# Kernel tuning notes

Measured on AMD Instinct MI355X. Metric: run time of the kernel, lower is better.

Reference implementation:

```python
import jax, jax.numpy as jnp
import numpy as np

N0, N1, N2 = 100000, 300000, 200000
C = 64
SLOPE = 0.2

NNZ_A0, NNZ_A1, NNZ_C2, NNZ_B1, NNZ_B2 = 600000, 1200000, 600000, 600000, 600000


def _seg_softmax(logits, seg, n):
    # softmax over nonzero entries of each row (segment = row index)
    m = jax.ops.segment_max(logits, seg, num_segments=n)
    e = jnp.exp(logits - m[seg])
    s = jax.ops.segment_sum(e, seg, num_segments=n)
    return e / s[seg]


def _hbs(x, rows, cols, W, a, n):
    # Higher-order attention block, same rank (m_hop=1, A values = 1)
    m = x @ W                                   # [n, out]
    out = W.shape[1]
    logits = jax.nn.leaky_relu((m @ a[:out])[rows] + (m @ a[out:])[cols], SLOPE)
    att = _seg_softmax(logits, rows, n)         # row-wise softmax on sparsity pattern
    return jax.ops.segment_sum(att[:, None] * m[cols], rows, num_segments=n)


def _hbns(xs, xt, t_rows, s_cols, Ws, Wt, a, n_s, n_t):
    # Higher-order attention block between ranks; neighborhood is [n_t, n_s]
    sm = xs @ Ws                                # [n_s, t_out]
    tm = xt @ Wt                                # [n_t, s_out]
    t_out, s_out = Ws.shape[1], Wt.shape[1]
    # e: source -> target attention logits (row = target); cat([sm_j, tm_i]) @ a
    e = jax.nn.leaky_relu((sm @ a[:t_out])[s_cols] + (tm @ a[t_out:])[t_rows], SLOPE)
    # f: target -> source attention logits (row = source); cat([tm_i, sm_j]) @ a
    f = jax.nn.leaky_relu((tm @ a[:s_out])[t_rows] + (sm @ a[s_out:])[s_cols], SLOPE)
    att_st = _seg_softmax(e, t_rows, n_t)
    att_ts = _seg_softmax(f, s_cols, n_s)
    msg_t = jax.ops.segment_sum(att_st[:, None] * sm[s_cols], t_rows, num_segments=n_t)
    msg_s = jax.ops.segment_sum(att_ts[:, None] * tm[t_rows], s_cols, num_segments=n_s)
    return msg_s, msg_t


def setup_inputs() -> dict:
    key = jax.random.key(0)
    ks = iter(jax.random.split(key, 64))
    sc = 1.0 / np.sqrt(C)
    d = {
        "x_0": jax.random.normal(next(ks), (N0, C), jnp.float32),
        "x_1": jax.random.normal(next(ks), (N1, C), jnp.float32),
        "x_2": jax.random.normal(next(ks), (N2, C), jnp.float32),
        "adj0_rows": jax.random.randint(next(ks), (NNZ_A0,), 0, N0, jnp.int32),
        "adj0_cols": jax.random.randint(next(ks), (NNZ_A0,), 0, N0, jnp.int32),
        "adj1_rows": jax.random.randint(next(ks), (NNZ_A1,), 0, N1, jnp.int32),
        "adj1_cols": jax.random.randint(next(ks), (NNZ_A1,), 0, N1, jnp.int32),
        "coadj2_rows": jax.random.randint(next(ks), (NNZ_C2,), 0, N2, jnp.int32),
        "coadj2_cols": jax.random.randint(next(ks), (NNZ_C2,), 0, N2, jnp.int32),
        "inc1_rows": jax.random.randint(next(ks), (NNZ_B1,), 0, N0, jnp.int32),
        "inc1_cols": jax.random.randint(next(ks), (NNZ_B1,), 0, N1, jnp.int32),
        "inc2_rows": jax.random.randint(next(ks), (NNZ_B2,), 0, N1, jnp.int32),
        "inc2_cols": jax.random.randint(next(ks), (NNZ_B2,), 0, N2, jnp.int32),
    }
    for nm in ["W_hbs0_l1", "W_hbs0_l2", "W_hbs1_l2", "W_hbs2_l2",
               "Ws01_l1", "Wt01_l1", "Ws12_l1", "Wt12_l1",
               "Ws01_l2", "Wt01_l2", "Ws12_l2", "Wt12_l2"]:
        d[nm] = jax.random.normal(next(ks), (C, C), jnp.float32) * sc
    for nm in ["a_hbs0_l1", "a_hbs0_l2", "a_hbs1_l2", "a_hbs2_l2",
               "a01_l1", "a12_l1", "a01_l2", "a12_l2"]:
        d[nm] = jax.random.normal(next(ks), (2 * C,), jnp.float32) * sc
    return d


def reference(x_0, x_1, x_2,
              adj0_rows, adj0_cols, adj1_rows, adj1_cols,
              coadj2_rows, coadj2_cols, inc1_rows, inc1_cols,
              inc2_rows, inc2_cols,
              W_hbs0_l1, a_hbs0_l1, W_hbs0_l2, a_hbs0_l2,
              W_hbs1_l2, a_hbs1_l2, W_hbs2_l2, a_hbs2_l2,
              Ws01_l1, Wt01_l1, a01_l1, Ws12_l1, Wt12_l1, a12_l1,
              Ws01_l2, Wt01_l2, a01_l2, Ws12_l2, Wt12_l2, a12_l2):
    # ---- level 1 ----
    x_0_to_0 = _hbs(x_0, adj0_rows, adj0_cols, W_hbs0_l1, a_hbs0_l1, N0)
    x_0_to_1, x_1_to_0 = _hbns(x_1, x_0, inc1_rows, inc1_cols,
                               Ws01_l1, Wt01_l1, a01_l1, N1, N0)
    x_1_to_2, x_2_to_1 = _hbns(x_2, x_1, inc2_rows, inc2_cols,
                               Ws12_l1, Wt12_l1, a12_l1, N2, N1)
    x_0_l1 = x_0_to_0 + x_1_to_0
    x_1_l1 = x_0_to_1 + x_2_to_1
    x_2_l1 = x_1_to_2
    # ---- level 2 ----
    x_0_to_0 = _hbs(x_0_l1, adj0_rows, adj0_cols, W_hbs0_l2, a_hbs0_l2, N0)
    x_1_to_1 = _hbs(x_1_l1, adj1_rows, adj1_cols, W_hbs1_l2, a_hbs1_l2, N1)
    x_2_to_2 = _hbs(x_2_l1, coadj2_rows, coadj2_cols, W_hbs2_l2, a_hbs2_l2, N2)
    x_0_to_1, _ = _hbns(x_1_l1, x_0_l1, inc1_rows, inc1_cols,
                        Ws01_l2, Wt01_l2, a01_l2, N1, N0)
    x_1_to_2, _ = _hbns(x_2_l1, x_1_l1, inc2_rows, inc2_cols,
                        Ws12_l2, Wt12_l2, a12_l2, N2, N1)
    x_0_out = x_0_to_0
    x_1_out = x_0_to_1 + x_1_to_1
    x_2_out = x_1_to_2 + x_2_to_2
    return x_0_out, x_1_out, x_2_out
```

## Files before the change

### kernel.cpp

```cpp
#include <hip/hip_runtime.h>

#define CN0 100000
#define CN1 300000
#define CN2 200000
#define EA0 600000
#define EA1 1200000
#define EC2 600000
#define EB1 600000
#define EB2 600000
#define TOTSEG (2*CN0 + 3*CN1 + 2*CN2)
#define TOTE   (EA0 + EA1 + EC2 + 2*EB1 + 2*EB2)

typedef __attribute__((ext_vector_type(8))) short short8;
typedef __attribute__((ext_vector_type(4))) float f32x4;
typedef __attribute__((ext_vector_type(4))) unsigned short u16x4;

__device__ __forceinline__ float lrelu(float v) { return v >= 0.f ? v : 0.2f * v; }
__device__ __forceinline__ unsigned short btop(float x) {
    return (unsigned short)(__float_as_uint(x) >> 16);
}
__device__ __forceinline__ unsigned short f2bf(float x) {
    unsigned u = __float_as_uint(x);
    return (unsigned short)((u + 0x7FFFu + ((u >> 16) & 1u)) >> 16);
}
__device__ __forceinline__ float bf2f(unsigned short b) {
    return __uint_as_float((unsigned)b << 16);
}

struct Pats {
    const int* seg[7];
    const int* vidx[7];
    int E[7];
    int base[7];
    int ebase[7];
};


__global__ void k_histrank(Pats P, int* __restrict__ rp1, int* __restrict__ rank) {
    int p = blockIdx.y;
    int e = blockIdx.x * blockDim.x + threadIdx.x;
    if (e >= P.E[p]) return;
    int gs = P.base[p] + P.seg[p][e];
    rank[P.ebase[p] + e] = atomicAdd(&rp1[gs], 1);
}

__global__ void k_blkscan(int* __restrict__ d, int n, int* __restrict__ bsum) {
    __shared__ int sh[256];
    int i = blockIdx.x * 256 + threadIdx.x;
    sh[threadIdx.x] = (i < n) ? d[i] : 0;
    __syncthreads();
    for (int off = 1; off < 256; off <<= 1) {
        int t = (threadIdx.x >= (unsigned)off) ? sh[threadIdx.x - off] : 0;
        __syncthreads();
        sh[threadIdx.x] += t;
        __syncthreads();
    }
    if (i < n) d[i] = sh[threadIdx.x];
    if (threadIdx.x == 255) bsum[blockIdx.x] = sh[255];
}

__global__ void k_scanb(int* __restrict__ bsum, int nb) {
    __shared__ int sh[256];
    __shared__ int carry;
    if (threadIdx.x == 0) carry = 0;
    __syncthreads();
    for (int base = 0; base < nb; base += 256) {
        int i = base + threadIdx.x;
        sh[threadIdx.x] = (i < nb) ? bsum[i] : 0;
        __syncthreads();
        for (int off = 1; off < 256; off <<= 1) {
            int t = (threadIdx.x >= (unsigned)off) ? sh[threadIdx.x - off] : 0;
            __syncthreads();
            sh[threadIdx.x] += t;
            __syncthreads();
        }
        if (i < nb) bsum[i] = sh[threadIdx.x] + carry;
        __syncthreads();
        if (threadIdx.x == 0) carry += sh[255];
        __syncthreads();
    }
}

__global__ void k_addoff(int* __restrict__ d, const int* __restrict__ bsum, int n) {
    int i = blockIdx.x * 256 + threadIdx.x;
    if (i < n && blockIdx.x > 0) d[i] += bsum[blockIdx.x - 1];
}

__global__ void k_place(Pats P, const int* __restrict__ rp, const int* __restrict__ rank,
                        int* __restrict__ vP) {
    int p = blockIdx.y;
    int e = blockIdx.x * blockDim.x + threadIdx.x;
    if (e >= P.E[p]) return;
    int gs = P.base[p] + P.seg[p][e];
    int pos = rp[gs] + rank[P.ebase[p] + e];
    vP[pos] = P.vidx[p][e];
}

__global__ void mm64_mfma(const float* __restrict__ X, const float* __restrict__ W,
                          const float* __restrict__ a, unsigned short* __restrict__ Yb,
                          float* __restrict__ p, float* __restrict__ q, int nchunk) {
    int lane = threadIdx.x & 63;
    int l15 = lane & 15, lq = lane >> 4;
    int wid = blockIdx.x * (blockDim.x >> 6) + (threadIdx.x >> 6);
    int nw = gridDim.x * (blockDim.x >> 6);

    short8 bh[4][2], bl[4][2];
#pragma unroll
    for (int t = 0; t < 4; ++t)
#pragma unroll
        for (int h = 0; h < 2; ++h) {
            const float* wp = W + (size_t)(h * 32 + lq * 8) * 64 + 16 * t + l15;
#pragma unroll
            for (int j = 0; j < 8; ++j) {
                float wv = wp[(size_t)j * 64];
                unsigned short hi = btop(wv);
                float rem = wv - __uint_as_float((unsigned)hi << 16);
                bh[t][h][j] = (short)hi;
                bl[t][h][j] = (short)btop(rem);
            }
        }
    float av0[4], av1[4];
#pragma unroll
    for (int t = 0; t < 4; ++t) {
        av0[t] = a[16 * t + l15];
        av1[t] = a[64 + 16 * t + l15];
    }

    for (int c = wid; c < nchunk; c += nw) {
        int base = c * 16;
        f32x4 acc[4];
#pragma unroll
        for (int t = 0; t < 4; ++t) acc[t] = (f32x4){0.f, 0.f, 0.f, 0.f};
#pragma unroll
        for (int h = 0; h < 2; ++h) {
            const f32x4* xp = (const f32x4*)(X + (size_t)(base + l15) * 64 + h * 32 + lq * 8);
            f32x4 x0 = xp[0], x1 = xp[1];
            short8 ah, al;
#pragma unroll
            for (int j = 0; j < 4; ++j) {
                unsigned short h0 = btop(x0[j]);
                float r0 = x0[j] - __uint_as_float((unsigned)h0 << 16);
                ah[j] = (short)h0;
                al[j] = (short)btop(r0);
                unsigned short h1 = btop(x1[j]);
                float r1 = x1[j] - __uint_as_float((unsigned)h1 << 16);
                ah[4 + j] = (short)h1;
                al[4 + j] = (short)btop(r1);
            }
#pragma unroll
            for (int t = 0; t < 4; ++t) {
                acc[t] = __builtin_amdgcn_mfma_f32_16x16x32_bf16(ah, bh[t][h], acc[t], 0, 0, 0);
                acc[t] = __builtin_amdgcn_mfma_f32_16x16x32_bf16(ah, bl[t][h], acc[t], 0, 0, 0);
                acc[t] = __builtin_amdgcn_mfma_f32_16x16x32_bf16(al, bh[t][h], acc[t], 0, 0, 0);
            }
        }
#pragma unroll
        for (int t = 0; t < 4; ++t)
#pragma unroll
            for (int r = 0; r < 4; ++r)
                Yb[(size_t)(base + lq * 4 + r) * 64 + 16 * t + l15] = f2bf(acc[t][r]);
#pragma unroll
        for (int r = 0; r < 4; ++r) {
            float pr = acc[0][r] * av0[0] + acc[1][r] * av0[1] + acc[2][r] * av0[2] + acc[3][r] * av0[3];
            float qr = acc[0][r] * av1[0] + acc[1][r] * av1[1] + acc[2][r] * av1[2] + acc[3][r] * av1[3];
#pragma unroll
            for (int off = 8; off; off >>= 1) {
                pr += __shfl_xor(pr, off, 64);
                qr += __shfl_xor(qr, off, 64);
            }
            if (l15 == 0) {
                p[base + lq * 4 + r] = pr;
                q[base + lq * 4 + r] = qr;
            }
        }
    }
}

__global__ void uvec_k(const float* __restrict__ W, const float* __restrict__ a2c,
                       float* __restrict__ uu) {
    int j = threadIdx.x;
    float s0 = 0.f, s1 = 0.f;
    for (int k = 0; k < 64; ++k) {
        float w = W[j * 64 + k];
        s0 = fmaf(w, a2c[k], s0);
        s1 = fmaf(w, a2c[64 + k], s1);
    }
    uu[j] = s0;
    uu[64 + j] = s1;
}

__global__ void proj2(const float* __restrict__ X, const float* __restrict__ uu,
                      float* __restrict__ p, float* __restrict__ q, int n) {
    int lane = threadIdx.x & 63;
    int row = blockIdx.x * (blockDim.x >> 6) + (threadIdx.x >> 6);
    if (row >= n) return;
    float xv = X[(size_t)row * 64 + lane];
    float a = xv * uu[lane];
    float b = xv * uu[64 + lane];
#pragma unroll
    for (int off = 32; off; off >>= 1) {
        a += __shfl_xor(a, off, 64);
        b += __shfl_xor(b, off, 64);
    }
    if (lane == 0) { p[row] = a; q[row] = b; }
}

__device__ __forceinline__ void seg_gather(
    const int* __restrict__ rp_all, int base, int s, const int* __restrict__ vP,
    const float* __restrict__ ps, const float* __restrict__ pv,
    const unsigned short* __restrict__ Mb, int gl, int gbase, f32x4& acc) {
    int gs = base + s;
    int beg = rp_all[gs];
    int end = rp_all[gs + 1];
    int nE = end - beg;
    if (nE <= 0) return;
    float pss = ps[s];
    if (nE <= 16) {
        int j = beg + gl;
        int v = (j < end) ? vP[j] : 0;
        float l = (j < end) ? lrelu(pss + pv[v]) : -3.4e38f;
        float mx = l;
#pragma unroll
        for (int off = 8; off; off >>= 1) mx = fmaxf(mx, __shfl_xor(mx, off, 64));
        float ev = (j < end) ? __expf(l - mx) : 0.f;
        float ssum = ev;
#pragma unroll
        for (int off = 8; off; off >>= 1) ssum += __shfl_xor(ssum, off, 64);
        float att = ev / ssum;
        for (int t0 = 0; t0 < nE; t0 += 4) {
            float w0 = __shfl(att, gbase + t0, 64), w1 = __shfl(att, gbase + t0 + 1, 64);
            float w2 = __shfl(att, gbase + t0 + 2, 64), w3 = __shfl(att, gbase + t0 + 3, 64);
            int u0 = __shfl(v, gbase + t0, 64), u1 = __shfl(v, gbase + t0 + 1, 64);
            int u2 = __shfl(v, gbase + t0 + 2, 64), u3 = __shfl(v, gbase + t0 + 3, 64);
            u16x4 m0 = *(const u16x4*)(Mb + (size_t)u0 * 64 + gl * 4);
            u16x4 m1 = *(const u16x4*)(Mb + (size_t)u1 * 64 + gl * 4);
            u16x4 m2 = *(const u16x4*)(Mb + (size_t)u2 * 64 + gl * 4);
            u16x4 m3 = *(const u16x4*)(Mb + (size_t)u3 * 64 + gl * 4);
#pragma unroll
            for (int kk = 0; kk < 4; ++kk)
                acc[kk] += w0 * bf2f(m0[kk]) + w1 * bf2f(m1[kk]) +
                           w2 * bf2f(m2[kk]) + w3 * bf2f(m3[kk]);
        }
    } else {
        float mx = -3.4e38f;
        for (int j0 = beg; j0 < end; j0 += 16) {
            int j = j0 + gl;
            float l = (j < end) ? lrelu(pss + pv[vP[j]]) : -3.4e38f;
            mx = fmaxf(mx, l);
        }
#pragma unroll
        for (int off = 8; off; off >>= 1) mx = fmaxf(mx, __shfl_xor(mx, off, 64));
        float ssum = 0.f;
        for (int j0 = beg; j0 < end; j0 += 16) {
            int j = j0 + gl;
            ssum += (j < end) ? __expf(lrelu(pss + pv[vP[j]]) - mx) : 0.f;
        }
#pragma unroll
        for (int off = 8; off; off >>= 1) ssum += __shfl_xor(ssum, off, 64);
        float inv = 1.f / ssum;
        for (int j0 = beg; j0 < end; j0 += 16) {
            int j = j0 + gl;
            int v = (j < end) ? vP[j] : 0;
            float ev = (j < end) ? __expf(lrelu(pss + pv[v]) - mx) * inv : 0.f;
            int cnt = min(16, end - j0);
            for (int t0 = 0; t0 < cnt; t0 += 4) {
                float w0 = __shfl(ev, gbase + t0, 64), w1 = __shfl(ev, gbase + t0 + 1, 64);
                float w2 = __shfl(ev, gbase + t0 + 2, 64), w3 = __shfl(ev, gbase + t0 + 3, 64);
                int u0 = __shfl(v, gbase + t0, 64), u1 = __shfl(v, gbase + t0 + 1, 64);
                int u2 = __shfl(v, gbase + t0 + 2, 64), u3 = __shfl(v, gbase + t0 + 3, 64);
                u16x4 m0 = *(const u16x4*)(Mb + (size_t)u0 * 64 + gl * 4);
                u16x4 m1 = *(const u16x4*)(Mb + (size_t)u1 * 64 + gl * 4);
                u16x4 m2 = *(const u16x4*)(Mb + (size_t)u2 * 64 + gl * 4);
                u16x4 m3 = *(const u16x4*)(Mb + (size_t)u3 * 64 + gl * 4);
#pragma unroll
                for (int kk = 0; kk < 4; ++kk)
                    acc[kk] += w0 * bf2f(m0[kk]) + w1 * bf2f(m1[kk]) +
                               w2 * bf2f(m2[kk]) + w3 * bf2f(m3[kk]);
            }
        }
    }
}

__global__ void k_attn1(const int* __restrict__ rp_all, int base, const int* __restrict__ vP,
                        const float* __restrict__ ps, const float* __restrict__ pv,
                        const unsigned short* __restrict__ Mb, float* __restrict__ out,
                        int nseg) {
    int lane = threadIdx.x & 63;
    int g = lane >> 4, gl = lane & 15, gbase = g << 4;
    int s = (blockIdx.x * (blockDim.x >> 6) + (threadIdx.x >> 6)) * 4 + g;
    if (s >= nseg) return;
    f32x4 acc = (f32x4){0.f, 0.f, 0.f, 0.f};
    seg_gather(rp_all, base, s, vP, ps, pv, Mb, gl, gbase, acc);
    *(f32x4*)(out + (size_t)s * 64 + gl * 4) = acc;
}

__global__ void k_attn2(const int* __restrict__ rp_all, int baseA, int baseB,
                        const int* __restrict__ vP,
                        const float* __restrict__ psA, const float* __restrict__ pvA,
                        const unsigned short* __restrict__ MbA,
                        const float* __restrict__ psB, const float* __restrict__ pvB,
                        const unsigned short* __restrict__ MbB,
                        float* __restrict__ out, int nseg) {
    int lane = threadIdx.x & 63;
    int g = lane >> 4, gl = lane & 15, gbase = g << 4;
    int s = (blockIdx.x * (blockDim.x >> 6) + (threadIdx.x >> 6)) * 4 + g;
    if (s >= nseg) return;
    f32x4 acc = (f32x4){0.f, 0.f, 0.f, 0.f};
    seg_gather(rp_all, baseA, s, vP, psA, pvA, MbA, gl, gbase, acc);
    seg_gather(rp_all, baseB, s, vP, psB, pvB, MbB, gl, gbase, acc);
    *(f32x4*)(out + (size_t)s * 64 + gl * 4) = acc;
}

extern "C" void kernel_launch(void* const* d_in, const int* in_sizes, int n_in,
                              void* d_out, int out_size, void* d_ws, size_t ws_size,
                              hipStream_t stream) {
    (void)in_sizes; (void)n_in; (void)ws_size; (void)out_size;
    const float* x0 = (const float*)d_in[0];
    const float* x1 = (const float*)d_in[1];
    const float* x2 = (const float*)d_in[2];
    const int* adj0r = (const int*)d_in[3];
    const int* adj0c = (const int*)d_in[4];
    const int* adj1r = (const int*)d_in[5];
    const int* adj1c = (const int*)d_in[6];
    const int* co2r = (const int*)d_in[7];
    const int* co2c = (const int*)d_in[8];
    const int* i1r = (const int*)d_in[9];
    const int* i1c = (const int*)d_in[10];
    const int* i2r = (const int*)d_in[11];
    const int* i2c = (const int*)d_in[12];
    const float* W_h0_l1 = (const float*)d_in[13];
    const float* W_h0_l2 = (const float*)d_in[14];
    const float* W_h1_l2 = (const float*)d_in[15];
    const float* W_h2_l2 = (const float*)d_in[16];
    const float* Ws01_l1 = (const float*)d_in[17];
    const float* Wt01_l1 = (const float*)d_in[18];
    const float* Ws12_l1 = (const float*)d_in[19];
    const float* Wt12_l1 = (const float*)d_in[20];
    const float* Ws01_l2 = (const float*)d_in[21];
    const float* Wt01_l2 = (const float*)d_in[22];
    const float* Ws12_l2 = (const float*)d_in[23];
    const float* Wt12_l2 = (const float*)d_in[24];
    const float* a_h0_l1 = (const float*)d_in[25];
    const float* a_h0_l2 = (const float*)d_in[26];
    const float* a_h1_l2 = (const float*)d_in[27];
    const float* a_h2_l2 = (const float*)d_in[28];
    const float* a01_l1 = (const float*)d_in[29];
    const float* a12_l1 = (const float*)d_in[30];
    const float* a01_l2 = (const float*)d_in[31];
    const float* a12_l2 = (const float*)d_in[32];

    float* fb = (float*)d_ws;
    float* t0 = fb;              float* t1 = t0 + 300000;
    float* t2 = t1 + 300000;     float* t3 = t2 + 300000;
    float* t4 = t3 + 300000;     float* t5 = t4 + 300000;
    float* t6 = t5 + 300000;     float* t7 = t6 + 300000;
    float* t8 = t7 + 300000;     float* t9 = t8 + 300000;
    float* t10 = t9 + 300000;    float* t11 = t10 + 300000;
    float* uu = t11 + 300000;
    unsigned short* YA = (unsigned short*)(uu + 128);
    unsigned short* YB = YA + (size_t)CN0 * 64;
    unsigned short* YC = YB + (size_t)CN1 * 64;
    unsigned short* YD = YC + (size_t)CN0 * 64;
    unsigned short* YE = YD + (size_t)CN2 * 64;
    int* rp_all = (int*)(YE + (size_t)CN1 * 64);
    int* vP_all = rp_all + (TOTSEG + 1);
    int* rank_all = vP_all + TOTE;
    int* bsum   = rank_all + TOTE;
    int* bsum2  = bsum + 6144;

    float* r0 = (float*)d_out;
    float* r1 = r0 + (size_t)CN0 * 64;
    float* r2 = r1 + (size_t)CN1 * 64;

    const int bA0 = 0;
    const int bE1 = CN0;
    const int bF1 = 2 * CN0;
    const int bE2 = 2 * CN0 + CN1;
    const int bF2 = 2 * CN0 + 2 * CN1;
    const int bA1 = 2 * CN0 + 2 * CN1 + CN2;
    const int bC2 = 2 * CN0 + 3 * CN1 + CN2;
    Pats P;
    P.seg[0] = adj0r; P.vidx[0] = adj0c; P.E[0] = EA0; P.base[0] = bA0;
    P.seg[1] = i1r;   P.vidx[1] = i1c;   P.E[1] = EB1; P.base[1] = bE1;
    P.seg[2] = i1c;   P.vidx[2] = i1r;   P.E[2] = EB1; P.base[2] = bF1;
    P.seg[3] = i2r;   P.vidx[3] = i2c;   P.E[3] = EB2; P.base[3] = bE2;
    P.seg[4] = i2c;   P.vidx[4] = i2r;   P.E[4] = EB2; P.base[4] = bF2;
    P.seg[5] = adj1r; P.vidx[5] = adj1c; P.E[5] = EA1; P.base[5] = bA1;
    P.seg[6] = co2r;  P.vidx[6] = co2c;  P.E[6] = EC2; P.base[6] = bC2;
    int eb = 0;
    for (int p = 0; p < 7; ++p) { P.ebase[p] = eb; eb += P.E[p]; }
    const int Emax = EA1;

    auto MMF = [&](const float* X, const float* W, const float* a, unsigned short* Yb,
                   float* p, float* q, int n) {
        int nchunk = n / 16;
        int blocks = min(1024, (nchunk + 3) / 4);
        mm64_mfma<<<dim3(blocks), dim3(256), 0, stream>>>(X, W, a, Yb, p, q, nchunk);
    };
    auto PROJ = [&](const float* X, const float* W, const float* a2, float* p, float* q, int n) {
        uvec_k<<<dim3(1), dim3(64), 0, stream>>>(W, a2, uu);
        proj2<<<dim3((n + 3) / 4), dim3(256), 0, stream>>>(X, uu, p, q, n);
    };
    auto AGG1 = [&](int base, const float* ps, const float* pv, const unsigned short* Mb,
                    float* out, int nseg) {
        k_attn1<<<dim3((nseg + 15) / 16), dim3(256), 0, stream>>>(
            rp_all, base, vP_all, ps, pv, Mb, out, nseg);
    };
    auto AGG2 = [&](int baseA, const float* psA, const float* pvA, const unsigned short* MbA,
                    int baseB, const float* psB, const float* pvB, const unsigned short* MbB,
                    float* out, int nseg) {
        k_attn2<<<dim3((nseg + 15) / 16), dim3(256), 0, stream>>>(
            rp_all, baseA, baseB, vP_all, psA, pvA, MbA, psB, pvB, MbB, out, nseg);
    };

    hipMemsetAsync(rp_all, 0, (size_t)(TOTSEG + 1) * 4, stream);
    {
        dim3 gh((Emax + 255) / 256, 7);
        k_histrank<<<gh, dim3(256), 0, stream>>>(P, rp_all + 1, rank_all);
        int nb = (TOTSEG + 255) / 256;
        int nb2 = (nb + 255) / 256;
        k_blkscan<<<dim3(nb), dim3(256), 0, stream>>>(rp_all + 1, TOTSEG, bsum);
        k_blkscan<<<dim3(nb2), dim3(256), 0, stream>>>(bsum, nb, bsum2);
        k_scanb<<<dim3(1), dim3(256), 0, stream>>>(bsum2, nb2);
        k_addoff<<<dim3(nb2), dim3(256), 0, stream>>>(bsum, bsum2, nb);
        k_addoff<<<dim3(nb), dim3(256), 0, stream>>>(rp_all + 1, bsum, TOTSEG);
        k_place<<<gh, dim3(256), 0, stream>>>(P, rp_all, rank_all, vP_all);
    }

    MMF(x0, W_h0_l1, a_h0_l1, YA, t0, t1, CN0);
    MMF(x1, Ws01_l1, a01_l1, YB, t2, t3, CN1);
    MMF(x0, Wt01_l1, a01_l1, YC, t4, t5, CN0);
    MMF(x2, Ws12_l1, a12_l1, YD, t6, t7, CN2);
    MMF(x1, Wt12_l1, a12_l1, YE, t8, t9, CN1);
    AGG2(bA0, t0, t1, YA, bE1, t5, t2, YB, r0, CN0);
    AGG2(bF1, t3, t4, YC, bE2, t9, t6, YD, r1, CN1);
    AGG1(bF2, t7, t8, YE, r2, CN2);

    MMF(r0, W_h0_l2, a_h0_l2, YA, t0, t1, CN0);
    MMF(r0, Wt01_l2, a01_l2, YC, t4, t11, CN0);
    MMF(r1, W_h1_l2, a_h1_l2, YB, t2, t3, CN1);
    MMF(r1, Wt12_l2, a12_l2, YE, t8, t11, CN1);
    PROJ(r1, Ws01_l2, a01_l2, t11, t6, CN1);
    MMF(r2, W_h2_l2, a_h2_l2, YD, t7, t9, CN2);
    PROJ(r2, Ws12_l2, a12_l2, t11, t10, CN2);
    AGG1(bA0, t0, t1, YA, r0, CN0);
    AGG2(bA1, t2, t3, YB, bF1, t6, t4, YC, r1, CN1);
    AGG2(bC2, t7, t9, YD, bF2, t10, t8, YE, r2, CN2);
}
```

Baseline: 899.0 us.

## Fuse level-1 matmuls with histogram and share input reads across level-2 projections

Merges the five level-1 projection matmuls and the CSR histogram/rank kernel into one launch with block roles, so independent work overlaps and launch overhead drops. At level 2, matmuls that read the same input are paired into one dual-weight kernel, and the separate projection pass is folded into the matmul input load, so each feature matrix is read once. The costs are higher register pressure in the dual kernel, a fixed 96-block budget per level-1 job, and role dispatch inside the fused kernel.

```diff
diff --git a/kernel.cpp b/kernel.cpp
--- a/kernel.cpp
+++ b/kernel.cpp
@@ -35,14 +35,116 @@
     int ebase[7];
 };
 
-
-__global__ void k_histrank(Pats P, int* __restrict__ rp1, int* __restrict__ rank) {
-    int p = blockIdx.y;
-    int e = blockIdx.x * blockDim.x + threadIdx.x;
-    if (e >= P.E[p]) return;
-    int gs = P.base[p] + P.seg[p][e];
-    rank[P.ebase[p] + e] = atomicAdd(&rp1[gs], 1);
-}
+struct MMJob {
+    const float* X; const float* W; const float* a;
+    unsigned short* Y; float* p; float* q; int nchunk;
+};
+
+__device__ __forceinline__ void mm_body(const float* __restrict__ X, const float* __restrict__ W,
+                                        const float* __restrict__ a, unsigned short* __restrict__ Yb,
+                                        float* __restrict__ p, float* __restrict__ q,
+                                        int nchunk, int wid, int nw, int lane) {
+    int l15 = lane & 15, lq = lane >> 4;
+    short8 bh[4][2], bl[4][2];
+#pragma unroll
+    for (int t = 0; t < 4; ++t)
+#pragma unroll
+        for (int h = 0; h < 2; ++h) {
+            const float* wp = W + (size_t)(h * 32 + lq * 8) * 64 + 16 * t + l15;
+#pragma unroll
+            for (int j = 0; j < 8; ++j) {
+                float wv = wp[(size_t)j * 64];
+                unsigned short hi = btop(wv);
+                float rem = wv - __uint_as_float((unsigned)hi << 16);
+                bh[t][h][j] = (short)hi;
+                bl[t][h][j] = (short)btop(rem);
+            }
+        }
+    float av0[4], av1[4];
+#pragma unroll
+    for (int t = 0; t < 4; ++t) {
+        av0[t] = a[16 * t + l15];
+        av1[t] = a[64 + 16 * t + l15];
+    }
+    for (int c = wid; c < nchunk; c += nw) {
+        int base = c * 16;
+        f32x4 acc[4];
+#pragma unroll
+        for (int t = 0; t < 4; ++t) acc[t] = (f32x4){0.f, 0.f, 0.f, 0.f};
+#pragma unroll
+        for (int h = 0; h < 2; ++h) {
+            const f32x4* xp = (const f32x4*)(X + (size_t)(base + l15) * 64 + h * 32 + lq * 8);
+            f32x4 x0 = xp[0], x1 = xp[1];
+            short8 ah, al;
+#pragma unroll
+            for (int j = 0; j < 4; ++j) {
+                unsigned short h0 = btop(x0[j]);
+                float r0 = x0[j] - __uint_as_float((unsigned)h0 << 16);
+                ah[j] = (short)h0;
+                al[j] = (short)btop(r0);
+                unsigned short h1 = btop(x1[j]);
+                float r1 = x1[j] - __uint_as_float((unsigned)h1 << 16);
+                ah[4 + j] = (short)h1;
+                al[4 + j] = (short)btop(r1);
+            }
+#pragma unroll
+            for (int t = 0; t < 4; ++t) {
+                acc[t] = __builtin_amdgcn_mfma_f32_16x16x32_bf16(ah, bh[t][h], acc[t], 0, 0, 0);
+                acc[t] = __builtin_amdgcn_mfma_f32_16x16x32_bf16(ah, bl[t][h], acc[t], 0, 0, 0);
+                acc[t] = __builtin_amdgcn_mfma_f32_16x16x32_bf16(al, bh[t][h], acc[t], 0, 0, 0);
+            }
+        }
+#pragma unroll
+        for (int t = 0; t < 4; ++t)
+#pragma unroll
+            for (int r = 0; r < 4; ++r)
+                Yb[(size_t)(base + lq * 4 + r) * 64 + 16 * t + l15] = f2bf(acc[t][r]);
+#pragma unroll
+        for (int r = 0; r < 4; ++r) {
+            float pr = acc[0][r] * av0[0] + acc[1][r] * av0[1] + acc[2][r] * av0[2] + acc[3][r] * av0[3];
+            float qr = acc[0][r] * av1[0] + acc[1][r] * av1[1] + acc[2][r] * av1[2] + acc[3][r] * av1[3];
+#pragma unroll
+            for (int off = 8; off; off >>= 1) {
+                pr += __shfl_xor(pr, off, 64);
+                qr += __shfl_xor(qr, off, 64);
+            }
+            if (l15 == 0) {
+                p[base + lq * 4 + r] = pr;
+                q[base + lq * 4 + r] = qr;
+            }
+        }
+    }
+}
+
+__global__ __launch_bounds__(256) void k_l1_fused(
+        MMJob j0, MMJob j1, MMJob j2, MMJob j3, MMJob j4,
+        Pats P, int* __restrict__ rp1, int* __restrict__ rank, int mmBlocks) {
+    int b = blockIdx.x;
+    int nm = 5 * mmBlocks;
+    int lane = threadIdx.x & 63;
+    if (b < nm) {
+        int role = b / mmBlocks, rb = b - role * mmBlocks;
+        MMJob J = (role == 0) ? j0 : (role == 1) ? j1 : (role == 2) ? j2
+                : (role == 3) ? j3 : j4;
+        int wid = rb * (blockDim.x >> 6) + (threadIdx.x >> 6);
+        int nw = mmBlocks * (blockDim.x >> 6);
+        mm_body(J.X, J.W, J.a, J.Y, J.p, J.q, J.nchunk, wid, nw, lane);
+    } else {
+        int hb = b - nm;
+        int pidx = 0, acc = 0;
+        for (; pidx < 7; ++pidx) {
+            int pb = (P.E[pidx] + 255) >> 8;
+            if (hb < acc + pb) break;
+            acc += pb;
+        }
+        if (pidx >= 7) return;
+        int e = (hb - acc) * 256 + threadIdx.x;
+        if (e >= P.E[pidx]) return;
+        int gs = P.base[pidx] + P.seg[pidx][e];
+        rank[P.ebase[pidx] + e] = atomicAdd(&rp1[gs], 1);
+    }
+}
+
 
 __global__ void k_blkscan(int* __restrict__ d, int n, int* __restrict__ bsum) {
     __shared__ int sh[256];
@@ -96,45 +198,83 @@
     vP[pos] = P.vidx[p][e];
 }
 
-__global__ void mm64_mfma(const float* __restrict__ X, const float* __restrict__ W,
-                          const float* __restrict__ a, unsigned short* __restrict__ Yb,
-                          float* __restrict__ p, float* __restrict__ q, int nchunk) {
+template <int DUAL, int VEC>
+__global__ __launch_bounds__(256) void mm64_t(
+        const float* __restrict__ X,
+        const float* __restrict__ W1, const float* __restrict__ a1,
+        unsigned short* __restrict__ Y1, float* __restrict__ p1, float* __restrict__ q1,
+        const float* __restrict__ W2, const float* __restrict__ a2,
+        unsigned short* __restrict__ Y2, float* __restrict__ p2, float* __restrict__ q2,
+        const float* __restrict__ uuv, float* __restrict__ pv, int nchunk) {
     int lane = threadIdx.x & 63;
     int l15 = lane & 15, lq = lane >> 4;
     int wid = blockIdx.x * (blockDim.x >> 6) + (threadIdx.x >> 6);
     int nw = gridDim.x * (blockDim.x >> 6);
 
-    short8 bh[4][2], bl[4][2];
+    short8 b1h[4][2], b1l[4][2], b2h[4][2], b2l[4][2];
 #pragma unroll
     for (int t = 0; t < 4; ++t)
 #pragma unroll
         for (int h = 0; h < 2; ++h) {
-            const float* wp = W + (size_t)(h * 32 + lq * 8) * 64 + 16 * t + l15;
+            const float* wp = W1 + (size_t)(h * 32 + lq * 8) * 64 + 16 * t + l15;
 #pragma unroll
             for (int j = 0; j < 8; ++j) {
                 float wv = wp[(size_t)j * 64];
                 unsigned short hi = btop(wv);
                 float rem = wv - __uint_as_float((unsigned)hi << 16);
-                bh[t][h][j] = (short)hi;
-                bl[t][h][j] = (short)btop(rem);
-            }
-        }
-    float av0[4], av1[4];
+                b1h[t][h][j] = (short)hi;
+                b1l[t][h][j] = (short)btop(rem);
+            }
+        }
+    if (DUAL) {
+#pragma unroll
+        for (int t = 0; t < 4; ++t)
+#pragma unroll
+            for (int h = 0; h < 2; ++h) {
+                const float* wp = W2 + (size_t)(h * 32 + lq * 8) * 64 + 16 * t + l15;
+#pragma unroll
+                for (int j = 0; j < 8; ++j) {
+                    float wv = wp[(size_t)j * 64];
+                    unsigned short hi = btop(wv);
+                    float rem = wv - __uint_as_float((unsigned)hi << 16);
+                    b2h[t][h][j] = (short)hi;
+                    b2l[t][h][j] = (short)btop(rem);
+                }
+            }
+    }
+    float a10[4], a11[4], a20[4], a21[4];
 #pragma unroll
     for (int t = 0; t < 4; ++t) {
-        av0[t] = a[16 * t + l15];
-        av1[t] = a[64 + 16 * t + l15];
+        a10[t] = a1[16 * t + l15];
+        a11[t] = a1[64 + 16 * t + l15];
+        if (DUAL) { a20[t] = a2[16 * t + l15]; a21[t] = a2[64 + 16 * t + l15]; }
+    }
+    float uv[16];
+    if (VEC) {
+#pragma unroll
+        for (int h = 0; h < 2; ++h)
+#pragma unroll
+            for (int j = 0; j < 8; ++j) uv[h * 8 + j] = uuv[h * 32 + lq * 8 + j];
     }
 
     for (int c = wid; c < nchunk; c += nw) {
         int base = c * 16;
-        f32x4 acc[4];
-#pragma unroll
-        for (int t = 0; t < 4; ++t) acc[t] = (f32x4){0.f, 0.f, 0.f, 0.f};
+        f32x4 acc1[4], acc2[4];
+#pragma unroll
+        for (int t = 0; t < 4; ++t) {
+            acc1[t] = (f32x4){0.f, 0.f, 0.f, 0.f};
+            if (DUAL) acc2[t] = (f32x4){0.f, 0.f, 0.f, 0.f};
+        }
+        float vp = 0.f;
 #pragma unroll
         for (int h = 0; h < 2; ++h) {
             const f32x4* xp = (const f32x4*)(X + (size_t)(base + l15) * 64 + h * 32 + lq * 8);
             f32x4 x0 = xp[0], x1 = xp[1];
+            if (VEC) {
+#pragma unroll
+                for (int j = 0; j < 4; ++j)
+                    vp += x0[j] * uv[h * 8 + j] + x1[j] * uv[h * 8 + 4 + j];
+            }
             short8 ah, al;
 #pragma unroll
             for (int j = 0; j < 4; ++j) {
@@ -149,29 +289,54 @@
             }
 #pragma unroll
             for (int t = 0; t < 4; ++t) {
-                acc[t] = __builtin_amdgcn_mfma_f32_16x16x32_bf16(ah, bh[t][h], acc[t], 0, 0, 0);
-                acc[t] = __builtin_amdgcn_mfma_f32_16x16x32_bf16(ah, bl[t][h], acc[t], 0, 0, 0);
-                acc[t] = __builtin_amdgcn_mfma_f32_16x16x32_bf16(al, bh[t][h], acc[t], 0, 0, 0);
+                acc1[t] = __builtin_amdgcn_mfma_f32_16x16x32_bf16(ah, b1h[t][h], acc1[t], 0, 0, 0);
+                acc1[t] = __builtin_amdgcn_mfma_f32_16x16x32_bf16(ah, b1l[t][h], acc1[t], 0, 0, 0);
+                acc1[t] = __builtin_amdgcn_mfma_f32_16x16x32_bf16(al, b1h[t][h], acc1[t], 0, 0, 0);
+                if (DUAL) {
+                    acc2[t] = __builtin_amdgcn_mfma_f32_16x16x32_bf16(ah, b2h[t][h], acc2[t], 0, 0, 0);
+                    acc2[t] = __builtin_amdgcn_mfma_f32_16x16x32_bf16(ah, b2l[t][h], acc2[t], 0, 0, 0);
+                    acc2[t] = __builtin_amdgcn_mfma_f32_16x16x32_bf16(al, b2h[t][h], acc2[t], 0, 0, 0);
+                }
             }
         }
 #pragma unroll
         for (int t = 0; t < 4; ++t)
 #pragma unroll
-            for (int r = 0; r < 4; ++r)
-                Yb[(size_t)(base + lq * 4 + r) * 64 + 16 * t + l15] = f2bf(acc[t][r]);
+            for (int r = 0; r < 4; ++r) {
+                Y1[(size_t)(base + lq * 4 + r) * 64 + 16 * t + l15] = f2bf(acc1[t][r]);
+                if (DUAL) Y2[(size_t)(base + lq * 4 + r) * 64 + 16 * t + l15] = f2bf(acc2[t][r]);
+            }
 #pragma unroll
         for (int r = 0; r < 4; ++r) {
-            float pr = acc[0][r] * av0[0] + acc[1][r] * av0[1] + acc[2][r] * av0[2] + acc[3][r] * av0[3];
-            float qr = acc[0][r] * av1[0] + acc[1][r] * av1[1] + acc[2][r] * av1[2] + acc[3][r] * av1[3];
+            float pr = acc1[0][r] * a10[0] + acc1[1][r] * a10[1] + acc1[2][r] * a10[2] + acc1[3][r] * a10[3];
+            float qr = acc1[0][r] * a11[0] + acc1[1][r] * a11[1] + acc1[2][r] * a11[2] + acc1[3][r] * a11[3];
 #pragma unroll
             for (int off = 8; off; off >>= 1) {
                 pr += __shfl_xor(pr, off, 64);
                 qr += __shfl_xor(qr, off, 64);
             }
             if (l15 == 0) {
-                p[base + lq * 4 + r] = pr;
-                q[base + lq * 4 + r] = qr;
-            }
+                p1[base + lq * 4 + r] = pr;
+                q1[base + lq * 4 + r] = qr;
+            }
+            if (DUAL) {
+                float pr2 = acc2[0][r] * a20[0] + acc2[1][r] * a20[1] + acc2[2][r] * a20[2] + acc2[3][r] * a20[3];
+                float qr2 = acc2[0][r] * a21[0] + acc2[1][r] * a21[1] + acc2[2][r] * a21[2] + acc2[3][r] * a21[3];
+#pragma unroll
+                for (int off = 8; off; off >>= 1) {
+                    pr2 += __shfl_xor(pr2, off, 64);
+                    qr2 += __shfl_xor(qr2, off, 64);
+                }
+                if (l15 == 0) {
+                    p2[base + lq * 4 + r] = pr2;
+                    q2[base + lq * 4 + r] = qr2;
+                }
+            }
+        }
+        if (VEC) {
+            vp += __shfl_xor(vp, 16, 64);
+            vp += __shfl_xor(vp, 32, 64);
+            if (lane < 16) pv[base + l15] = vp;
         }
     }
 }
@@ -187,22 +352,6 @@
     }
     uu[j] = s0;
     uu[64 + j] = s1;
-}
-
-__global__ void proj2(const float* __restrict__ X, const float* __restrict__ uu,
-                      float* __restrict__ p, float* __restrict__ q, int n) {
-    int lane = threadIdx.x & 63;
-    int row = blockIdx.x * (blockDim.x >> 6) + (threadIdx.x >> 6);
-    if (row >= n) return;
-    float xv = X[(size_t)row * 64 + lane];
-    float a = xv * uu[lane];
-    float b = xv * uu[64 + lane];
-#pragma unroll
-    for (int off = 32; off; off >>= 1) {
-        a += __shfl_xor(a, off, 64);
-        b += __shfl_xor(b, off, 64);
-    }
-    if (lane == 0) { p[row] = a; q[row] = b; }
 }
 
 __device__ __forceinline__ void seg_gather(
@@ -356,8 +505,9 @@
     float* t6 = t5 + 300000;     float* t7 = t6 + 300000;
     float* t8 = t7 + 300000;     float* t9 = t8 + 300000;
     float* t10 = t9 + 300000;    float* t11 = t10 + 300000;
-    float* uu = t11 + 300000;
-    unsigned short* YA = (unsigned short*)(uu + 128);
+    float* uuA = t11 + 300000;
+    float* uuB = uuA + 128;
+    unsigned short* YA = (unsigned short*)(uuB + 128);
     unsigned short* YB = YA + (size_t)CN0 * 64;
     unsigned short* YC = YB + (size_t)CN1 * 64;
     unsigned short* YD = YC + (size_t)CN0 * 64;
@@ -387,20 +537,14 @@
     P.seg[4] = i2c;   P.vidx[4] = i2r;   P.E[4] = EB2; P.base[4] = bF2;
     P.seg[5] = adj1r; P.vidx[5] = adj1c; P.E[5] = EA1; P.base[5] = bA1;
     P.seg[6] = co2r;  P.vidx[6] = co2c;  P.E[6] = EC2; P.base[6] = bC2;
-    int eb = 0;
-    for (int p = 0; p < 7; ++p) { P.ebase[p] = eb; eb += P.E[p]; }
+    int eb = 0, histBlocks = 0;
+    for (int p = 0; p < 7; ++p) {
+        P.ebase[p] = eb;
+        eb += P.E[p];
+        histBlocks += (P.E[p] + 255) / 256;
+    }
     const int Emax = EA1;
 
-    auto MMF = [&](const float* X, const float* W, const float* a, unsigned short* Yb,
-                   float* p, float* q, int n) {
-        int nchunk = n / 16;
-        int blocks = min(1024, (nchunk + 3) / 4);
-        mm64_mfma<<<dim3(blocks), dim3(256), 0, stream>>>(X, W, a, Yb, p, q, nchunk);
-    };
-    auto PROJ = [&](const float* X, const float* W, const float* a2, float* p, float* q, int n) {
-        uvec_k<<<dim3(1), dim3(64), 0, stream>>>(W, a2, uu);
-        proj2<<<dim3((n + 3) / 4), dim3(256), 0, stream>>>(X, uu, p, q, n);
-    };
     auto AGG1 = [&](int base, const float* ps, const float* pv, const unsigned short* Mb,
                     float* out, int nseg) {
         k_attn1<<<dim3((nseg + 15) / 16), dim3(256), 0, stream>>>(
@@ -415,8 +559,16 @@
 
     hipMemsetAsync(rp_all, 0, (size_t)(TOTSEG + 1) * 4, stream);
     {
-        dim3 gh((Emax + 255) / 256, 7);
-        k_histrank<<<gh, dim3(256), 0, stream>>>(P, rp_all + 1, rank_all);
+        const int mmBlocks = 96;
+        MMJob j0 = {x0, W_h0_l1, a_h0_l1, YA, t0, t1, CN0 / 16};
+        MMJob j1 = {x1, Ws01_l1, a01_l1, YB, t2, t3, CN1 / 16};
+        MMJob j2 = {x0, Wt01_l1, a01_l1, YC, t4, t5, CN0 / 16};
+        MMJob j3 = {x2, Ws12_l1, a12_l1, YD, t6, t7, CN2 / 16};
+        MMJob j4 = {x1, Wt12_l1, a12_l1, YE, t8, t9, CN1 / 16};
+        k_l1_fused<<<dim3(5 * mmBlocks + histBlocks), dim3(256), 0, stream>>>(
+            j0, j1, j2, j3, j4, P, rp_all + 1, rank_all, mmBlocks);
+    }
+    {
         int nb = (TOTSEG + 255) / 256;
         int nb2 = (nb + 255) / 256;
         k_blkscan<<<dim3(nb), dim3(256), 0, stream>>>(rp_all + 1, TOTSEG, bsum);
@@ -424,25 +576,30 @@
         k_scanb<<<dim3(1), dim3(256), 0, stream>>>(bsum2, nb2);
         k_addoff<<<dim3(nb2), dim3(256), 0, stream>>>(bsum, bsum2, nb);
         k_addoff<<<dim3(nb), dim3(256), 0, stream>>>(rp_all + 1, bsum, TOTSEG);
+        dim3 gh((Emax + 255) / 256, 7);
         k_place<<<gh, dim3(256), 0, stream>>>(P, rp_all, rank_all, vP_all);
     }
 
-    MMF(x0, W_h0_l1, a_h0_l1, YA, t0, t1, CN0);
-    MMF(x1, Ws01_l1, a01_l1, YB, t2, t3, CN1);
-    MMF(x0, Wt01_l1, a01_l1, YC, t4, t5, CN0);
-    MMF(x2, Ws12_l1, a12_l1, YD, t6, t7, CN2);
-    MMF(x1, Wt12_l1, a12_l1, YE, t8, t9, CN1);
     AGG2(bA0, t0, t1, YA, bE1, t5, t2, YB, r0, CN0);
     AGG2(bF1, t3, t4, YC, bE2, t9, t6, YD, r1, CN1);
     AGG1(bF2, t7, t8, YE, r2, CN2);
 
-    MMF(r0, W_h0_l2, a_h0_l2, YA, t0, t1, CN0);
-    MMF(r0, Wt01_l2, a01_l2, YC, t4, t11, CN0);
-    MMF(r1, W_h1_l2, a_h1_l2, YB, t2, t3, CN1);
-    MMF(r1, Wt12_l2, a12_l2, YE, t8, t11, CN1);
-    PROJ(r1, Ws01_l2, a01_l2, t11, t6, CN1);
-    MMF(r2, W_h2_l2, a_h2_l2, YD, t7, t9, CN2);
-    PROJ(r2, Ws12_l2, a12_l2, t11, t10, CN2);
+    uvec_k<<<dim3(1), dim3(64), 0, stream>>>(Ws01_l2, a01_l2, uuA);
+    uvec_k<<<dim3(1), dim3(64), 0, stream>>>(Ws12_l2, a12_l2, uuB);
+    {
+        int blocks0 = min(1024, (CN0 / 16 + 3) / 4);
+        int blocks1 = min(1024, (CN1 / 16 + 3) / 4);
+        int blocks2 = min(1024, (CN2 / 16 + 3) / 4);
+        mm64_t<1, 0><<<dim3(blocks0), dim3(256), 0, stream>>>(
+            r0, W_h0_l2, a_h0_l2, YA, t0, t1,
+            Wt01_l2, a01_l2, YC, t4, t11, nullptr, nullptr, CN0 / 16);
+        mm64_t<1, 1><<<dim3(blocks1), dim3(256), 0, stream>>>(
+            r1, W_h1_l2, a_h1_l2, YB, t2, t3,
+            Wt12_l2, a12_l2, YE, t8, t11, uuA + 64, t6, CN1 / 16);
+        mm64_t<0, 1><<<dim3(blocks2), dim3(256), 0, stream>>>(
+            r2, W_h2_l2, a_h2_l2, YD, t7, t9,
+            nullptr, nullptr, nullptr, nullptr, nullptr, uuB + 64, t10, CN2 / 16);
+    }
     AGG1(bA0, t0, t1, YA, r0, CN0);
     AGG2(bA1, t2, t3, YB, bF1, t6, t4, YC, r1, CN1);
     AGG2(bC2, t7, t9, YD, bF2, t10, t8, YE, r2, CN2);
```

Result: faster. 816.0 us (-9.2%).
